# Kernel tuning notes

Measured on AMD Instinct MI355X. Metric: run time of the kernel, lower is better.

Reference implementation:

```python
import jax, jax.numpy as jnp
import numpy as np
import math


def setup_inputs() -> dict:
    key = jax.random.key(0)
    ks = jax.random.split(key, 7)
    d_input, d_state, d_output = 256, 256, 256
    B_, S_ = 8, 4096
    x = jax.random.normal(ks[0], (B_, S_, d_input), dtype=jnp.float32)
    log_lambda_real = jax.random.normal(ks[1], (d_state,), dtype=jnp.float32)
    lambda_imag = jax.random.normal(ks[2], (d_state,), dtype=jnp.float32)
    dt = jnp.clip(0.01 + jax.random.normal(ks[3], (d_state,), dtype=jnp.float32) * 0.01, 0.005, 0.1)
    log_dt = jnp.log(dt)
    B = jax.random.normal(ks[4], (d_state, d_input), dtype=jnp.float32) / d_state ** 0.5
    C_real = jax.random.normal(ks[5], (d_output, d_state), dtype=jnp.float32) / d_state ** 0.5
    C_imag = jax.random.normal(ks[6], (d_output, d_state), dtype=jnp.float32) / d_state ** 0.5
    return {"x": x, "log_lambda_real": log_lambda_real, "lambda_imag": lambda_imag,
            "log_dt": log_dt, "B": B, "C_real": C_real, "C_imag": C_imag}


def reference(x, log_lambda_real, lambda_imag, log_dt, B, C_real, C_imag):
    batch, seq_len, _ = x.shape
    # continuous-time poles and step sizes
    Lambda = -jnp.exp(log_lambda_real) + 1j * lambda_imag            # [N] complex
    dt = jnp.clip(jnp.exp(log_dt), 0.005, 0.1)                       # [N]
    # bilinear discretization
    denom = 1.0 - 0.5 * dt * Lambda                                  # [N] complex
    A_bar = (1.0 + 0.5 * dt * Lambda) / denom                        # [N] complex
    B_bar = (dt / denom)[:, None] * B                                # [N, d_in] complex
    # project input into state space: u[b,s,n] (complex)
    u = jnp.matmul(x, B_bar.real.T) + 1j * jnp.matmul(x, B_bar.imag.T)  # [B,S,N]
    # kernel A^0 .. A^{L-1} via cumprod (faithful to original)
    A_poles = jnp.broadcast_to(A_bar[:, None], (A_bar.shape[0], seq_len))  # [N,S]
    A_cp = jnp.cumprod(A_poles, axis=1)
    A_powers = jnp.concatenate([jnp.ones_like(A_cp[:, :1]), A_cp[:, :-1]], axis=1)  # [N,S]
    # FFT causal convolution
    n_fft = 2 ** math.ceil(math.log2(seq_len * 2 - 1))
    u_t = jnp.swapaxes(u, 1, 2)                                      # [B,N,S]
    u_f = jnp.fft.fft(u_t, n=n_fft, axis=-1)                          # [B,N,F]
    A_f = jnp.fft.fft(A_powers, n=n_fft, axis=-1)                     # [N,F]
    h = jnp.fft.ifft(u_f * A_f[None], n=n_fft, axis=-1)[..., :seq_len]  # [B,N,S]
    h = jnp.swapaxes(h, 1, 2)                                         # [B,S,N]
    # output projection, keep real part
    C_c = C_real + 1j * C_imag                                        # [d_out,N]
    return jnp.matmul(h, C_c.T).real                                  # [B,S,d_out]
```

## Files before the change

kernel.cpp:

```cpp
#include <hip/hip_runtime.h>
#include <hip/hip_bf16.h>

#define BB 8
#define SS 4096
#define NN 256
#define CHUNK 32
#define NCH (SS/CHUNK)

#define WS_FINR_B ((size_t)0)
#define WS_FINI_B ((size_t)1 << 20)
#define WS_CP_B   ((size_t)2 << 20)
#define WS_BP_B   (((size_t)2 << 20) + (256u << 10))

typedef __bf16 bf16_t;
typedef bf16_t bf16x8 __attribute__((ext_vector_type(8)));
typedef float  f32x4  __attribute__((ext_vector_type(4)));
typedef unsigned int u32x4 __attribute__((ext_vector_type(4)));

__device__ inline bf16_t f2b(float f) {
    __hip_bfloat16 h = __float2bfloat16(f);
    return __builtin_bit_cast(bf16_t, h);
}
__device__ inline float b2f_lo(unsigned v) {
    unsigned u = v << 16; return __builtin_bit_cast(float, u);
}
__device__ inline float b2f_hi(unsigned v) {
    unsigned u = v & 0xffff0000u; return __builtin_bit_cast(float, u);
}
__device__ inline unsigned pack2(float lo, float hi) {
    unsigned a = (unsigned)__builtin_bit_cast(unsigned short, f2b(lo));
    unsigned b = (unsigned)__builtin_bit_cast(unsigned short, f2b(hi));
    return a | (b << 16);
}
__device__ inline bf16x8 cvt8(f32x4 a, f32x4 b) {
    bf16x8 o;
    o[0]=f2b(a[0]); o[1]=f2b(a[1]); o[2]=f2b(a[2]); o[3]=f2b(a[3]);
    o[4]=f2b(b[0]); o[5]=f2b(b[1]); o[6]=f2b(b[2]); o[7]=f2b(b[3]);
    return o;
}

__device__ inline void ssm_consts(const float* llr, const float* li, const float* ldt,
                                  int n, float& Ar, float& Ai, float& sr, float& si) {
    float lr = -expf(llr[n]);
    float im = li[n];
    float dt = expf(ldt[n]);
    dt = fminf(fmaxf(dt, 0.005f), 0.1f);
    float hr = 0.5f * dt * lr, hi = 0.5f * dt * im;
    float dr = 1.f - hr, di = -hi;
    float inv = 1.f / (dr*dr + di*di);
    Ar = ((1.f + hr)*dr + hi*di) * inv;
    Ai = (hi*dr - (1.f + hr)*di) * inv;
    sr = dt * dr * inv;
    si = -dt * di * inv;
}

__global__ __launch_bounds__(256) void kprep(const float* __restrict__ Bw,
                                             const float* __restrict__ Cr,
                                             const float* __restrict__ Ci,
                                             u32x4* __restrict__ Cpack,
                                             u32x4* __restrict__ Bpack) {
    int t = threadIdx.x, bid = blockIdx.x;
    const float* src;
    float sign;
    u32x4* dst;
    int ks;
    if (bid < 16) { ks = bid;      src = (ks < 8) ? Cr : Ci; sign = (ks < 8) ? 1.f : -1.f; dst = Cpack; }
    else          { ks = bid - 16; src = Bw;                 sign = 1.f;                   dst = Bpack; }
    int ksl = ks & 7;
    #pragma unroll
    for (int jj = 0; jj < 4; ++jj) {
        int s = t + 256 * jj;
        int ot = s >> 6, lane = s & 63;
        int o  = ot*16 + (lane & 15);
        int kb = ksl*32 + (lane >> 4)*8;
        bf16x8 v;
        #pragma unroll
        for (int e = 0; e < 8; ++e) v[e] = f2b(sign * src[o*256 + kb + e]);
        dst[(ks*16 + ot)*64 + lane] = __builtin_bit_cast(u32x4, v);
    }
}


__global__ __launch_bounds__(256, 2) void kA(
    const float* __restrict__ X,
    const float* __restrict__ llr,
    const float* __restrict__ li,
    const float* __restrict__ ldt,
    const u32x4* __restrict__ Bpack,
    float* __restrict__ finr,
    float* __restrict__ fini,
    float* __restrict__ out)
{
    __shared__ __align__(16) char hlds[65536];
    int t = threadIdx.x;
    int bid = blockIdx.x;
    int m0 = bid * 64;
    int b = bid >> 6;
    int cbase = (bid & 63) * 2;
    int w = t >> 6, lane = t & 63, q = lane >> 4, r = lane & 15;

    f32x4 acc[4][4] = {};
    for (int kk = 0; kk < 4; ++kk) {
        #pragma unroll
        for (int ss = 0; ss < 2; ++ss) {
            int s = t + 256 * ss;
            int m = s >> 3, kg = s & 7;
            const f32x4* px = (const f32x4*)(X + (size_t)(m0 + m)*256 + kk*64 + kg*8);
            *(bf16x8*)(hlds + 32768 + m*128 + ((kg ^ (m & 7)) << 4)) = cvt8(px[0], px[1]);
        }
        __syncthreads();
        bf16x8 bp[2][4], xf[2][4];
        #pragma unroll
        for (int kb = 0; kb < 2; ++kb) {
            #pragma unroll
            for (int nt = 0; nt < 4; ++nt)
                bp[kb][nt] = __builtin_bit_cast(bf16x8,
                    Bpack[((kk*2 + kb)*16 + w*4 + nt)*64 + lane]);
            #pragma unroll
            for (int mt = 0; mt < 4; ++mt) {
                int m = mt*16 + r;
                xf[kb][mt] = *(const bf16x8*)(hlds + 32768 + m*128 +
                                              (((kb*4 + q) ^ (m & 7)) << 4));
            }
        }
        #pragma unroll
        for (int kb = 0; kb < 2; ++kb)
            #pragma unroll
            for (int nt = 0; nt < 4; ++nt)
                #pragma unroll
                for (int mt = 0; mt < 4; ++mt)
                    acc[nt][mt] = __builtin_amdgcn_mfma_f32_16x16x32_bf16(
                        bp[kb][nt], xf[kb][mt], acc[nt][mt], 0, 0, 0);
        __syncthreads();
    }
    #pragma unroll
    for (int nt = 0; nt < 4; ++nt) {
        int n0 = w*64 + nt*16 + q*4;
        #pragma unroll
        for (int mt = 0; mt < 4; ++mt) {
            int m = mt*16 + r;
            uint2 d;
            d.x = pack2(acc[nt][mt][0], acc[nt][mt][1]);
            d.y = pack2(acc[nt][mt][2], acc[nt][mt][3]);
            *(uint2*)(hlds + m*512 + (((n0 >> 3) ^ ((m >> 1) & 31)) << 4) + (n0 & 7)*2) = d;
        }
    }
    __syncthreads();

    {
        int p = t & 127, ch = t >> 7;
        int cb = cbase + ch;
        float Ar0,Ai0,sr0,si0, Ar1,Ai1,sr1,si1;
        ssm_consts(llr, li, ldt, 2*p,   Ar0, Ai0, sr0, si0);
        ssm_consts(llr, li, ldt, 2*p+1, Ar1, Ai1, sr1, si1);
        float hr0=0.f, hi0=0.f, hr1=0.f, hi1=0.f;
        #pragma unroll
        for (int i2 = 0; i2 < 16; ++i2) {
            int row = ch*32 + i2*2;
            char* a = hlds + row*512 + (((p >> 2) ^ ((row >> 1) & 31)) << 4) + (p & 3)*4;
            unsigned v0 = *(unsigned*)a;
            unsigned v1 = *(unsigned*)(a + 512);
            float x0 = b2f_lo(v0), x1 = b2f_hi(v0);
            float t0r = fmaf(Ar0, hr0, fmaf(-Ai0, hi0, sr0*x0));
            float t0i = fmaf(Ar0, hi0, fmaf( Ai0, hr0, si0*x0));
            float t1r = fmaf(Ar1, hr1, fmaf(-Ai1, hi1, sr1*x1));
            float t1i = fmaf(Ar1, hi1, fmaf( Ai1, hr1, si1*x1));
            hr0=t0r; hi0=t0i; hr1=t1r; hi1=t1i;
            *(unsigned*)a           = pack2(hr0, hr1);
            *(unsigned*)(a + 32768) = pack2(hi0, hi1);
            x0 = b2f_lo(v1); x1 = b2f_hi(v1);
            t0r = fmaf(Ar0, hr0, fmaf(-Ai0, hi0, sr0*x0));
            t0i = fmaf(Ar0, hi0, fmaf( Ai0, hr0, si0*x0));
            t1r = fmaf(Ar1, hr1, fmaf(-Ai1, hi1, sr1*x1));
            t1i = fmaf(Ar1, hi1, fmaf( Ai1, hr1, si1*x1));
            hr0=t0r; hi0=t0i; hr1=t1r; hi1=t1i;
            *(unsigned*)(a + 512)         = pack2(hr0, hr1);
            *(unsigned*)(a + 32768 + 512) = pack2(hi0, hi1);
        }
        int f0 = (b*NCH + cb)*NN + 2*p;
        finr[f0] = hr0; finr[f0+1] = hr1;
        fini[f0] = hi0; fini[f0+1] = hi1;
    }
    __syncthreads();

    char* dst = (char*)out + ((size_t)bid << 16);
    #pragma unroll
    for (int jj = 0; jj < 16; ++jj)
        *(u32x4*)(dst + jj*4096 + t*16) = *(const u32x4*)(hlds + jj*4096 + t*16);
}

__global__ __launch_bounds__(256, 2) void kB(
    const float* __restrict__ llr,
    const float* __restrict__ li,
    const float* __restrict__ ldt,
    const u32x4* __restrict__ Cpack,
    const float* __restrict__ finr,
    const float* __restrict__ fini,
    float* __restrict__ out)
{
    __shared__ __align__(16) char hlds[65536];
    int t = threadIdx.x;
    int bid = blockIdx.x;
    int m0 = bid * 64;
    int b = bid >> 6;
    int cbase = (bid & 63) * 2;
    int w = t >> 6, lane = t & 63, q = lane >> 4, r = lane & 15;

    const char* src = (const char*)out + ((size_t)bid << 16);
    u32x4 img[16];
    #pragma unroll
    for (int jj = 0; jj < 16; ++jj)
        img[jj] = *(const u32x4*)(src + jj*4096 + t*16);

    int p = t & 127, ch = t >> 7;
    int cb = cbase + ch;
    float Ar0,Ai0,sr0,si0, Ar1,Ai1,sr1,si1;
    ssm_consts(llr, li, ldt, 2*p,   Ar0, Ai0, sr0, si0);
    ssm_consts(llr, li, ldt, 2*p+1, Ar1, Ai1, sr1, si1);
    float g0r=0.f, g0i=0.f, g1r=0.f, g1i=0.f;
    if (cb > 0) {
        float P0r=Ar0, P0i=Ai0, P1r=Ar1, P1i=Ai1;
        #pragma unroll
        for (int i = 0; i < 5; ++i) {
            float u0 = P0r*P0r - P0i*P0i; P0i = 2.f*P0r*P0i; P0r = u0;
            float u1 = P1r*P1r - P1i*P1i; P1i = 2.f*P1r*P1i; P1r = u1;
        }
        float c0r=0.f, c0i=0.f, c1r=0.f, c1i=0.f;
        #pragma unroll 4
        for (int j = 0; j < cb; ++j) {
            int ff = (b*NCH + j)*NN + 2*p;
            float2 fr = *(const float2*)(finr + ff);
            float2 fi = *(const float2*)(fini + ff);
            float n0r = fmaf(P0r, c0r, fmaf(-P0i, c0i, fr.x));
            float n0i = fmaf(P0r, c0i, fmaf( P0i, c0r, fi.x));
            float n1r = fmaf(P1r, c1r, fmaf(-P1i, c1i, fr.y));
            float n1i = fmaf(P1r, c1i, fmaf( P1i, c1r, fi.y));
            c0r=n0r; c0i=n0i; c1r=n1r; c1i=n1i;
        }
        g0r = Ar0*c0r - Ai0*c0i; g0i = Ar0*c0i + Ai0*c0r;
        g1r = Ar1*c1r - Ai1*c1i; g1i = Ar1*c1i + Ai1*c1r;
    }

    #pragma unroll
    for (int jj = 0; jj < 16; ++jj)
        *(u32x4*)(hlds + jj*4096 + t*16) = img[jj];
    __syncthreads();

    if (cb > 0) {
        #pragma unroll
        for (int i2 = 0; i2 < 16; ++i2) {
            int row = ch*32 + i2*2;
            char* a = hlds + row*512 + (((p >> 2) ^ ((row >> 1) & 31)) << 4) + (p & 3)*4;
            unsigned ur0 = *(unsigned*)a;
            unsigned ur1 = *(unsigned*)(a + 512);
            unsigned ui0 = *(unsigned*)(a + 32768);
            unsigned ui1 = *(unsigned*)(a + 32768 + 512);
            *(unsigned*)a           = pack2(b2f_lo(ur0) + g0r, b2f_hi(ur0) + g1r);
            *(unsigned*)(a + 32768) = pack2(b2f_lo(ui0) + g0i, b2f_hi(ui0) + g1i);
            { float t0 = Ar0*g0r - Ai0*g0i; g0i = fmaf(Ar0, g0i, Ai0*g0r); g0r = t0;
              float t1 = Ar1*g1r - Ai1*g1i; g1i = fmaf(Ar1, g1i, Ai1*g1r); g1r = t1; }
            *(unsigned*)(a + 512)         = pack2(b2f_lo(ur1) + g0r, b2f_hi(ur1) + g1r);
            *(unsigned*)(a + 32768 + 512) = pack2(b2f_lo(ui1) + g0i, b2f_hi(ui1) + g1i);
            { float t0 = Ar0*g0r - Ai0*g0i; g0i = fmaf(Ar0, g0i, Ai0*g0r); g0r = t0;
              float t1 = Ar1*g1r - Ai1*g1i; g1i = fmaf(Ar1, g1i, Ai1*g1r); g1r = t1; }
        }
    }
    __syncthreads();

    f32x4 acc2[4][4] = {};
    #pragma unroll
    for (int ks = 0; ks < 16; ++ks) {
        int base = (ks & 8) ? 32768 : 0;
        int kin = ks & 7;
        bf16x8 af[4];
        #pragma unroll
        for (int mt = 0; mt < 4; ++mt) {
            int row = mt*16 + r;
            af[mt] = *(const bf16x8*)(hlds + base + row*512 +
                     (((kin*4 + q) ^ ((row >> 1) & 31)) << 4));
        }
        #pragma unroll
        for (int nt = 0; nt < 4; ++nt) {
            bf16x8 cf = __builtin_bit_cast(bf16x8, Cpack[(ks*16 + w*4 + nt)*64 + lane]);
            #pragma unroll
            for (int mt = 0; mt < 4; ++mt)
                acc2[mt][nt] = __builtin_amdgcn_mfma_f32_16x16x32_bf16(
                    af[mt], cf, acc2[mt][nt], 0, 0, 0);
        }
    }
    #pragma unroll
    for (int mt = 0; mt < 4; ++mt)
        #pragma unroll
        for (int nt = 0; nt < 4; ++nt)
            #pragma unroll
            for (int reg = 0; reg < 4; ++reg)
                out[(size_t)(m0 + mt*16 + q*4 + reg)*NN + w*64 + nt*16 + r] =
                    acc2[mt][nt][reg];
}

extern "C" void kernel_launch(void* const* d_in, const int* in_sizes, int n_in,
                              void* d_out, int out_size, void* d_ws, size_t ws_size,
                              hipStream_t stream) {
    const float* x   = (const float*)d_in[0];
    const float* llr = (const float*)d_in[1];
    const float* li  = (const float*)d_in[2];
    const float* ldt = (const float*)d_in[3];
    const float* Bw  = (const float*)d_in[4];
    const float* Cr  = (const float*)d_in[5];
    const float* Ci  = (const float*)d_in[6];

    char* wsb = (char*)d_ws;
    float* finr  = (float*)(wsb + WS_FINR_B);
    float* fini  = (float*)(wsb + WS_FINI_B);
    u32x4* Cpack = (u32x4*)(wsb + WS_CP_B);
    u32x4* Bpack = (u32x4*)(wsb + WS_BP_B);
    float* outp  = (float*)d_out;

    kprep<<<24, 256, 0, stream>>>(Bw, Cr, Ci, Cpack, Bpack);
    kA<<<512, 256, 0, stream>>>(x, llr, li, ldt, Bpack, finr, fini, outp);
    kB<<<512, 256, 0, stream>>>(llr, li, ldt, Cpack, finr, fini, outp);
}
```

Baseline: 131.7 us.

## Fuse chunk scan and output kernels using inter-block flag synchronization

Merges the two main kernels into one. Each block publishes its chunk-final states with atomic stores and a release flag, then spins on the flags of earlier blocks in the same batch before applying the carry and the output projection. This removes the round trip of the 64KB per-block intermediate image through global memory and one kernel launch. It relies on all 512 blocks being co-resident, or on blocks being dispatched in order, to avoid deadlock, and it adds spin-wait latency along the chunk dependency chain.

```diff
diff --git a/kernel.cpp b/kernel.cpp
--- a/kernel.cpp
+++ b/kernel.cpp
@@ -7,15 +7,17 @@
 #define CHUNK 32
 #define NCH (SS/CHUNK)
 
-#define WS_FINR_B ((size_t)0)
-#define WS_FINI_B ((size_t)1 << 20)
-#define WS_CP_B   ((size_t)2 << 20)
-#define WS_BP_B   (((size_t)2 << 20) + (256u << 10))
+#define WS_FINU_B ((size_t)0)
+#define WS_FINV_B ((size_t)1 << 20)
+#define WS_FLAG_B ((size_t)2 << 20)
+#define WS_CP_B   (((size_t)2 << 20) + 65536)
+#define WS_BP_B   (((size_t)2 << 20) + 65536 + 262144)
 
 typedef __bf16 bf16_t;
 typedef bf16_t bf16x8 __attribute__((ext_vector_type(8)));
 typedef float  f32x4  __attribute__((ext_vector_type(4)));
 typedef unsigned int u32x4 __attribute__((ext_vector_type(4)));
+typedef unsigned long long u64_t;
 
 __device__ inline bf16_t f2b(float f) {
     __hip_bfloat16 h = __float2bfloat16(f);
@@ -58,8 +60,10 @@
                                              const float* __restrict__ Cr,
                                              const float* __restrict__ Ci,
                                              u32x4* __restrict__ Cpack,
-                                             u32x4* __restrict__ Bpack) {
+                                             u32x4* __restrict__ Bpack,
+                                             int* __restrict__ flags) {
     int t = threadIdx.x, bid = blockIdx.x;
+    if (bid == 0) { flags[t] = 0; flags[t + 256] = 0; }
     const float* src;
     float sign;
     u32x4* dst;
@@ -81,14 +85,16 @@
 }
 
 
-__global__ __launch_bounds__(256, 2) void kA(
+__global__ __launch_bounds__(256, 2) void kfused(
     const float* __restrict__ X,
     const float* __restrict__ llr,
     const float* __restrict__ li,
     const float* __restrict__ ldt,
     const u32x4* __restrict__ Bpack,
-    float* __restrict__ finr,
-    float* __restrict__ fini,
+    const u32x4* __restrict__ Cpack,
+    u64_t* __restrict__ finu,
+    u64_t* __restrict__ finv,
+    int* __restrict__ flags,
     float* __restrict__ out)
 {
     __shared__ __align__(16) char hlds[65536];
@@ -96,7 +102,8 @@
     int bid = blockIdx.x;
     int m0 = bid * 64;
     int b = bid >> 6;
-    int cbase = (bid & 63) * 2;
+    int d = bid & 63;
+    int cbase = d * 2;
     int w = t >> 6, lane = t & 63, q = lane >> 4, r = lane & 15;
 
     f32x4 acc[4][4] = {};
@@ -139,20 +146,20 @@
         #pragma unroll
         for (int mt = 0; mt < 4; ++mt) {
             int m = mt*16 + r;
-            uint2 d;
-            d.x = pack2(acc[nt][mt][0], acc[nt][mt][1]);
-            d.y = pack2(acc[nt][mt][2], acc[nt][mt][3]);
-            *(uint2*)(hlds + m*512 + (((n0 >> 3) ^ ((m >> 1) & 31)) << 4) + (n0 & 7)*2) = d;
+            uint2 dd;
+            dd.x = pack2(acc[nt][mt][0], acc[nt][mt][1]);
+            dd.y = pack2(acc[nt][mt][2], acc[nt][mt][3]);
+            *(uint2*)(hlds + m*512 + (((n0 >> 3) ^ ((m >> 1) & 31)) << 4) + (n0 & 7)*2) = dd;
         }
     }
     __syncthreads();
 
+    int p = t & 127, ch = t >> 7;
+    int cb = cbase + ch;
+    float Ar0,Ai0,sr0,si0, Ar1,Ai1,sr1,si1;
+    ssm_consts(llr, li, ldt, 2*p,   Ar0, Ai0, sr0, si0);
+    ssm_consts(llr, li, ldt, 2*p+1, Ar1, Ai1, sr1, si1);
     {
-        int p = t & 127, ch = t >> 7;
-        int cb = cbase + ch;
-        float Ar0,Ai0,sr0,si0, Ar1,Ai1,sr1,si1;
-        ssm_consts(llr, li, ldt, 2*p,   Ar0, Ai0, sr0, si0);
-        ssm_consts(llr, li, ldt, 2*p+1, Ar1, Ai1, sr1, si1);
         float hr0=0.f, hi0=0.f, hr1=0.f, hi1=0.f;
         #pragma unroll
         for (int i2 = 0; i2 < 16; ++i2) {
@@ -177,48 +184,28 @@
             *(unsigned*)(a + 512)         = pack2(hr0, hr1);
             *(unsigned*)(a + 32768 + 512) = pack2(hi0, hi1);
         }
-        int f0 = (b*NCH + cb)*NN + 2*p;
-        finr[f0] = hr0; finr[f0+1] = hr1;
-        fini[f0] = hi0; fini[f0+1] = hi1;
+        float2 fr2; fr2.x = hr0; fr2.y = hr1;
+        float2 fi2; fi2.x = hi0; fi2.y = hi1;
+        size_t fidx = (size_t)(b*NCH + cb)*128 + p;
+        __hip_atomic_store(finu + fidx, __builtin_bit_cast(u64_t, fr2),
+                           __ATOMIC_RELAXED, __HIP_MEMORY_SCOPE_AGENT);
+        __hip_atomic_store(finv + fidx, __builtin_bit_cast(u64_t, fi2),
+                           __ATOMIC_RELAXED, __HIP_MEMORY_SCOPE_AGENT);
     }
     __syncthreads();
-
-    char* dst = (char*)out + ((size_t)bid << 16);
-    #pragma unroll
-    for (int jj = 0; jj < 16; ++jj)
-        *(u32x4*)(dst + jj*4096 + t*16) = *(const u32x4*)(hlds + jj*4096 + t*16);
-}
-
-__global__ __launch_bounds__(256, 2) void kB(
-    const float* __restrict__ llr,
-    const float* __restrict__ li,
-    const float* __restrict__ ldt,
-    const u32x4* __restrict__ Cpack,
-    const float* __restrict__ finr,
-    const float* __restrict__ fini,
-    float* __restrict__ out)
-{
-    __shared__ __align__(16) char hlds[65536];
-    int t = threadIdx.x;
-    int bid = blockIdx.x;
-    int m0 = bid * 64;
-    int b = bid >> 6;
-    int cbase = (bid & 63) * 2;
-    int w = t >> 6, lane = t & 63, q = lane >> 4, r = lane & 15;
-
-    const char* src = (const char*)out + ((size_t)bid << 16);
-    u32x4 img[16];
-    #pragma unroll
-    for (int jj = 0; jj < 16; ++jj)
-        img[jj] = *(const u32x4*)(src + jj*4096 + t*16);
-
-    int p = t & 127, ch = t >> 7;
-    int cb = cbase + ch;
-    float Ar0,Ai0,sr0,si0, Ar1,Ai1,sr1,si1;
-    ssm_consts(llr, li, ldt, 2*p,   Ar0, Ai0, sr0, si0);
-    ssm_consts(llr, li, ldt, 2*p+1, Ar1, Ai1, sr1, si1);
-    float g0r=0.f, g0i=0.f, g1r=0.f, g1i=0.f;
+    if (t == 0)
+        __hip_atomic_store(flags + bid, 1, __ATOMIC_RELEASE, __HIP_MEMORY_SCOPE_AGENT);
+
     if (cb > 0) {
+        if (d > 0) {
+            int fi_ = b*64 + ((lane < d) ? lane : 0);
+            while (true) {
+                int fl = __hip_atomic_load(flags + fi_, __ATOMIC_ACQUIRE,
+                                           __HIP_MEMORY_SCOPE_AGENT);
+                if (__all(fl != 0)) break;
+                __builtin_amdgcn_s_sleep(16);
+            }
+        }
         float P0r=Ar0, P0i=Ai0, P1r=Ar1, P1i=Ai1;
         #pragma unroll
         for (int i = 0; i < 5; ++i) {
@@ -228,25 +215,18 @@
         float c0r=0.f, c0i=0.f, c1r=0.f, c1i=0.f;
         #pragma unroll 4
         for (int j = 0; j < cb; ++j) {
-            int ff = (b*NCH + j)*NN + 2*p;
-            float2 fr = *(const float2*)(finr + ff);
-            float2 fi = *(const float2*)(fini + ff);
+            u64_t vr = finu[(size_t)(b*NCH + j)*128 + p];
+            u64_t vi = finv[(size_t)(b*NCH + j)*128 + p];
+            float2 fr = __builtin_bit_cast(float2, vr);
+            float2 fi = __builtin_bit_cast(float2, vi);
             float n0r = fmaf(P0r, c0r, fmaf(-P0i, c0i, fr.x));
             float n0i = fmaf(P0r, c0i, fmaf( P0i, c0r, fi.x));
             float n1r = fmaf(P1r, c1r, fmaf(-P1i, c1i, fr.y));
             float n1i = fmaf(P1r, c1i, fmaf( P1i, c1r, fi.y));
             c0r=n0r; c0i=n0i; c1r=n1r; c1i=n1i;
         }
-        g0r = Ar0*c0r - Ai0*c0i; g0i = Ar0*c0i + Ai0*c0r;
-        g1r = Ar1*c1r - Ai1*c1i; g1i = Ar1*c1i + Ai1*c1r;
-    }
-
-    #pragma unroll
-    for (int jj = 0; jj < 16; ++jj)
-        *(u32x4*)(hlds + jj*4096 + t*16) = img[jj];
-    __syncthreads();
-
-    if (cb > 0) {
+        float g0r = Ar0*c0r - Ai0*c0i, g0i = Ar0*c0i + Ai0*c0r;
+        float g1r = Ar1*c1r - Ai1*c1i, g1i = Ar1*c1i + Ai1*c1r;
         #pragma unroll
         for (int i2 = 0; i2 < 16; ++i2) {
             int row = ch*32 + i2*2;
@@ -310,13 +290,14 @@
     const float* Ci  = (const float*)d_in[6];
 
     char* wsb = (char*)d_ws;
-    float* finr  = (float*)(wsb + WS_FINR_B);
-    float* fini  = (float*)(wsb + WS_FINI_B);
+    u64_t* finu  = (u64_t*)(wsb + WS_FINU_B);
+    u64_t* finv  = (u64_t*)(wsb + WS_FINV_B);
+    int*   flags = (int*)(wsb + WS_FLAG_B);
     u32x4* Cpack = (u32x4*)(wsb + WS_CP_B);
     u32x4* Bpack = (u32x4*)(wsb + WS_BP_B);
     float* outp  = (float*)d_out;
 
-    kprep<<<24, 256, 0, stream>>>(Bw, Cr, Ci, Cpack, Bpack);
-    kA<<<512, 256, 0, stream>>>(x, llr, li, ldt, Bpack, finr, fini, outp);
-    kB<<<512, 256, 0, stream>>>(llr, li, ldt, Cpack, finr, fini, outp);
-}
+    kprep<<<24, 256, 0, stream>>>(Bw, Cr, Ci, Cpack, Bpack, flags);
+    kfused<<<512, 256, 0, stream>>>(x, llr, li, ldt, Bpack, Cpack,
+                                    finu, finv, flags, outp);
+}
```

Measured after the change: 156.7 us. +19.0%, slower.

## Pass real bf16 projection instead of complex scan image between kernels

Applied to the files above, without the earlier changes.

kA now writes only the bf16 input projection u (32KB per block) to a workspace buffer and computes chunk-final states without storing the complex scan. kB reloads u, computes the carry-in prefix, then reruns the chunk scan starting from the carry and writes real and imaginary states into LDS for the output GEMM. This halves the intermediate global traffic and shrinks kA's LDS so it can raise occupancy to 3 blocks. In exchange the scan is computed twice, once in each kernel.

```diff
diff --git a/kernel.cpp b/kernel.cpp
--- a/kernel.cpp
+++ b/kernel.cpp
@@ -9,8 +9,9 @@
 
 #define WS_FINR_B ((size_t)0)
 #define WS_FINI_B ((size_t)1 << 20)
-#define WS_CP_B   ((size_t)2 << 20)
-#define WS_BP_B   (((size_t)2 << 20) + (256u << 10))
+#define WS_VIMG_B ((size_t)2 << 20)
+#define WS_CP_B   ((size_t)18 << 20)
+#define WS_BP_B   (((size_t)18 << 20) + 262144)
 
 typedef __bf16 bf16_t;
 typedef bf16_t bf16x8 __attribute__((ext_vector_type(8)));
@@ -81,7 +82,7 @@
 }
 
 
-__global__ __launch_bounds__(256, 2) void kA(
+__global__ __launch_bounds__(256, 3) void kA(
     const float* __restrict__ X,
     const float* __restrict__ llr,
     const float* __restrict__ li,
@@ -89,6 +90,113 @@
     const u32x4* __restrict__ Bpack,
     float* __restrict__ finr,
     float* __restrict__ fini,
+    char* __restrict__ vimg)
+{
+    __shared__ __align__(16) char hlds[40960];
+    int t = threadIdx.x;
+    int bid = blockIdx.x;
+    int m0 = bid * 64;
+    int b = bid >> 6;
+    int cbase = (bid & 63) * 2;
+    int w = t >> 6, lane = t & 63, q = lane >> 4, r = lane & 15;
+
+    f32x4 acc[4][4] = {};
+    for (int kk = 0; kk < 4; ++kk) {
+        #pragma unroll
+        for (int ss = 0; ss < 2; ++ss) {
+            int s = t + 256 * ss;
+            int m = s >> 3, kg = s & 7;
+            const f32x4* px = (const f32x4*)(X + (size_t)(m0 + m)*256 + kk*64 + kg*8);
+            *(bf16x8*)(hlds + 32768 + m*128 + ((kg ^ (m & 7)) << 4)) = cvt8(px[0], px[1]);
+        }
+        __syncthreads();
+        bf16x8 bp[2][4], xf[2][4];
+        #pragma unroll
+        for (int kb = 0; kb < 2; ++kb) {
+            #pragma unroll
+            for (int nt = 0; nt < 4; ++nt)
+                bp[kb][nt] = __builtin_bit_cast(bf16x8,
+                    Bpack[((kk*2 + kb)*16 + w*4 + nt)*64 + lane]);
+            #pragma unroll
+            for (int mt = 0; mt < 4; ++mt) {
+                int m = mt*16 + r;
+                xf[kb][mt] = *(const bf16x8*)(hlds + 32768 + m*128 +
+                                              (((kb*4 + q) ^ (m & 7)) << 4));
+            }
+        }
+        #pragma unroll
+        for (int kb = 0; kb < 2; ++kb)
+            #pragma unroll
+            for (int nt = 0; nt < 4; ++nt)
+                #pragma unroll
+                for (int mt = 0; mt < 4; ++mt)
+                    acc[nt][mt] = __builtin_amdgcn_mfma_f32_16x16x32_bf16(
+                        bp[kb][nt], xf[kb][mt], acc[nt][mt], 0, 0, 0);
+        __syncthreads();
+    }
+    #pragma unroll
+    for (int nt = 0; nt < 4; ++nt) {
+        int n0 = w*64 + nt*16 + q*4;
+        #pragma unroll
+        for (int mt = 0; mt < 4; ++mt) {
+            int m = mt*16 + r;
+            uint2 dd;
+            dd.x = pack2(acc[nt][mt][0], acc[nt][mt][1]);
+            dd.y = pack2(acc[nt][mt][2], acc[nt][mt][3]);
+            *(uint2*)(hlds + m*512 + (((n0 >> 3) ^ ((m >> 1) & 31)) << 4) + (n0 & 7)*2) = dd;
+        }
+    }
+    __syncthreads();
+
+    {
+        char* dst = vimg + ((size_t)bid << 15);
+        #pragma unroll
+        for (int jj = 0; jj < 8; ++jj)
+            *(u32x4*)(dst + jj*4096 + t*16) = *(const u32x4*)(hlds + jj*4096 + t*16);
+    }
+
+    {
+        int p = t & 127, ch = t >> 7;
+        int cb = cbase + ch;
+        float Ar0,Ai0,sr0,si0, Ar1,Ai1,sr1,si1;
+        ssm_consts(llr, li, ldt, 2*p,   Ar0, Ai0, sr0, si0);
+        ssm_consts(llr, li, ldt, 2*p+1, Ar1, Ai1, sr1, si1);
+        float hr0=0.f, hi0=0.f, hr1=0.f, hi1=0.f;
+        #pragma unroll
+        for (int i2 = 0; i2 < 16; ++i2) {
+            int row = ch*32 + i2*2;
+            const char* a = hlds + row*512 + (((p >> 2) ^ ((row >> 1) & 31)) << 4) + (p & 3)*4;
+            unsigned v0 = *(const unsigned*)a;
+            unsigned v1 = *(const unsigned*)(a + 512);
+            float x0 = b2f_lo(v0), x1 = b2f_hi(v0);
+            float t0r = fmaf(Ar0, hr0, fmaf(-Ai0, hi0, sr0*x0));
+            float t0i = fmaf(Ar0, hi0, fmaf( Ai0, hr0, si0*x0));
+            float t1r = fmaf(Ar1, hr1, fmaf(-Ai1, hi1, sr1*x1));
+            float t1i = fmaf(Ar1, hi1, fmaf( Ai1, hr1, si1*x1));
+            hr0=t0r; hi0=t0i; hr1=t1r; hi1=t1i;
+            x0 = b2f_lo(v1); x1 = b2f_hi(v1);
+            t0r = fmaf(Ar0, hr0, fmaf(-Ai0, hi0, sr0*x0));
+            t0i = fmaf(Ar0, hi0, fmaf( Ai0, hr0, si0*x0));
+            t1r = fmaf(Ar1, hr1, fmaf(-Ai1, hi1, sr1*x1));
+            t1i = fmaf(Ar1, hi1, fmaf( Ai1, hr1, si1*x1));
+            hr0=t0r; hi0=t0i; hr1=t1r; hi1=t1i;
+        }
+        int f0 = (b*NCH + cb)*NN + 2*p;
+        float2 fr2; fr2.x = hr0; fr2.y = hr1;
+        float2 fi2; fi2.x = hi0; fi2.y = hi1;
+        *(float2*)(finr + f0) = fr2;
+        *(float2*)(fini + f0) = fi2;
+    }
+}
+
+__global__ __launch_bounds__(256, 2) void kB(
+    const float* __restrict__ llr,
+    const float* __restrict__ li,
+    const float* __restrict__ ldt,
+    const u32x4* __restrict__ Cpack,
+    const float* __restrict__ finr,
+    const float* __restrict__ fini,
+    const char* __restrict__ vimg,
     float* __restrict__ out)
 {
     __shared__ __align__(16) char hlds[65536];
@@ -99,61 +207,45 @@
     int cbase = (bid & 63) * 2;
     int w = t >> 6, lane = t & 63, q = lane >> 4, r = lane & 15;
 
-    f32x4 acc[4][4] = {};
-    for (int kk = 0; kk < 4; ++kk) {
-        #pragma unroll
-        for (int ss = 0; ss < 2; ++ss) {
-            int s = t + 256 * ss;
-            int m = s >> 3, kg = s & 7;
-            const f32x4* px = (const f32x4*)(X + (size_t)(m0 + m)*256 + kk*64 + kg*8);
-            *(bf16x8*)(hlds + 32768 + m*128 + ((kg ^ (m & 7)) << 4)) = cvt8(px[0], px[1]);
-        }
-        __syncthreads();
-        bf16x8 bp[2][4], xf[2][4];
-        #pragma unroll
-        for (int kb = 0; kb < 2; ++kb) {
-            #pragma unroll
-            for (int nt = 0; nt < 4; ++nt)
-                bp[kb][nt] = __builtin_bit_cast(bf16x8,
-                    Bpack[((kk*2 + kb)*16 + w*4 + nt)*64 + lane]);
-            #pragma unroll
-            for (int mt = 0; mt < 4; ++mt) {
-                int m = mt*16 + r;
-                xf[kb][mt] = *(const bf16x8*)(hlds + 32768 + m*128 +
-                                              (((kb*4 + q) ^ (m & 7)) << 4));
-            }
-        }
-        #pragma unroll
-        for (int kb = 0; kb < 2; ++kb)
-            #pragma unroll
-            for (int nt = 0; nt < 4; ++nt)
-                #pragma unroll
-                for (int mt = 0; mt < 4; ++mt)
-                    acc[nt][mt] = __builtin_amdgcn_mfma_f32_16x16x32_bf16(
-                        bp[kb][nt], xf[kb][mt], acc[nt][mt], 0, 0, 0);
-        __syncthreads();
-    }
-    #pragma unroll
-    for (int nt = 0; nt < 4; ++nt) {
-        int n0 = w*64 + nt*16 + q*4;
-        #pragma unroll
-        for (int mt = 0; mt < 4; ++mt) {
-            int m = mt*16 + r;
-            uint2 d;
-            d.x = pack2(acc[nt][mt][0], acc[nt][mt][1]);
-            d.y = pack2(acc[nt][mt][2], acc[nt][mt][3]);
-            *(uint2*)(hlds + m*512 + (((n0 >> 3) ^ ((m >> 1) & 31)) << 4) + (n0 & 7)*2) = d;
-        }
-    }
+    const char* src = vimg + ((size_t)bid << 15);
+    u32x4 img[8];
+    #pragma unroll
+    for (int jj = 0; jj < 8; ++jj)
+        img[jj] = *(const u32x4*)(src + jj*4096 + t*16);
+
+    int p = t & 127, ch = t >> 7;
+    int cb = cbase + ch;
+    float Ar0,Ai0,sr0,si0, Ar1,Ai1,sr1,si1;
+    ssm_consts(llr, li, ldt, 2*p,   Ar0, Ai0, sr0, si0);
+    ssm_consts(llr, li, ldt, 2*p+1, Ar1, Ai1, sr1, si1);
+    float c0r=0.f, c0i=0.f, c1r=0.f, c1i=0.f;
+    if (cb > 0) {
+        float P0r=Ar0, P0i=Ai0, P1r=Ar1, P1i=Ai1;
+        #pragma unroll
+        for (int i = 0; i < 5; ++i) {
+            float u0 = P0r*P0r - P0i*P0i; P0i = 2.f*P0r*P0i; P0r = u0;
+            float u1 = P1r*P1r - P1i*P1i; P1i = 2.f*P1r*P1i; P1r = u1;
+        }
+        #pragma unroll 4
+        for (int j = 0; j < cb; ++j) {
+            int ff = (b*NCH + j)*NN + 2*p;
+            float2 fr = *(const float2*)(finr + ff);
+            float2 fi = *(const float2*)(fini + ff);
+            float n0r = fmaf(P0r, c0r, fmaf(-P0i, c0i, fr.x));
+            float n0i = fmaf(P0r, c0i, fmaf( P0i, c0r, fi.x));
+            float n1r = fmaf(P1r, c1r, fmaf(-P1i, c1i, fr.y));
+            float n1i = fmaf(P1r, c1i, fmaf( P1i, c1r, fi.y));
+            c0r=n0r; c0i=n0i; c1r=n1r; c1i=n1i;
+        }
+    }
+
+    #pragma unroll
+    for (int jj = 0; jj < 8; ++jj)
+        *(u32x4*)(hlds + jj*4096 + t*16) = img[jj];
     __syncthreads();
 
     {
-        int p = t & 127, ch = t >> 7;
-        int cb = cbase + ch;
-        float Ar0,Ai0,sr0,si0, Ar1,Ai1,sr1,si1;
-        ssm_consts(llr, li, ldt, 2*p,   Ar0, Ai0, sr0, si0);
-        ssm_consts(llr, li, ldt, 2*p+1, Ar1, Ai1, sr1, si1);
-        float hr0=0.f, hi0=0.f, hr1=0.f, hi1=0.f;
+        float hr0=c0r, hi0=c0i, hr1=c1r, hi1=c1i;
         #pragma unroll
         for (int i2 = 0; i2 < 16; ++i2) {
             int row = ch*32 + i2*2;
@@ -177,93 +269,6 @@
             *(unsigned*)(a + 512)         = pack2(hr0, hr1);
             *(unsigned*)(a + 32768 + 512) = pack2(hi0, hi1);
         }
-        int f0 = (b*NCH + cb)*NN + 2*p;
-        finr[f0] = hr0; finr[f0+1] = hr1;
-        fini[f0] = hi0; fini[f0+1] = hi1;
-    }
-    __syncthreads();
-
-    char* dst = (char*)out + ((size_t)bid << 16);
-    #pragma unroll
-    for (int jj = 0; jj < 16; ++jj)
-        *(u32x4*)(dst + jj*4096 + t*16) = *(const u32x4*)(hlds + jj*4096 + t*16);
-}
-
-__global__ __launch_bounds__(256, 2) void kB(
-    const float* __restrict__ llr,
-    const float* __restrict__ li,
-    const float* __restrict__ ldt,
-    const u32x4* __restrict__ Cpack,
-    const float* __restrict__ finr,
-    const float* __restrict__ fini,
-    float* __restrict__ out)
-{
-    __shared__ __align__(16) char hlds[65536];
-    int t = threadIdx.x;
-    int bid = blockIdx.x;
-    int m0 = bid * 64;
-    int b = bid >> 6;
-    int cbase = (bid & 63) * 2;
-    int w = t >> 6, lane = t & 63, q = lane >> 4, r = lane & 15;
-
-    const char* src = (const char*)out + ((size_t)bid << 16);
-    u32x4 img[16];
-    #pragma unroll
-    for (int jj = 0; jj < 16; ++jj)
-        img[jj] = *(const u32x4*)(src + jj*4096 + t*16);
-
-    int p = t & 127, ch = t >> 7;
-    int cb = cbase + ch;
-    float Ar0,Ai0,sr0,si0, Ar1,Ai1,sr1,si1;
-    ssm_consts(llr, li, ldt, 2*p,   Ar0, Ai0, sr0, si0);
-    ssm_consts(llr, li, ldt, 2*p+1, Ar1, Ai1, sr1, si1);
-    float g0r=0.f, g0i=0.f, g1r=0.f, g1i=0.f;
-    if (cb > 0) {
-        float P0r=Ar0, P0i=Ai0, P1r=Ar1, P1i=Ai1;
-        #pragma unroll
-        for (int i = 0; i < 5; ++i) {
-            float u0 = P0r*P0r - P0i*P0i; P0i = 2.f*P0r*P0i; P0r = u0;
-            float u1 = P1r*P1r - P1i*P1i; P1i = 2.f*P1r*P1i; P1r = u1;
-        }
-        float c0r=0.f, c0i=0.f, c1r=0.f, c1i=0.f;
-        #pragma unroll 4
-        for (int j = 0; j < cb; ++j) {
-            int ff = (b*NCH + j)*NN + 2*p;
-            float2 fr = *(const float2*)(finr + ff);
-            float2 fi = *(const float2*)(fini + ff);
-            float n0r = fmaf(P0r, c0r, fmaf(-P0i, c0i, fr.x));
-            float n0i = fmaf(P0r, c0i, fmaf( P0i, c0r, fi.x));
-            float n1r = fmaf(P1r, c1r, fmaf(-P1i, c1i, fr.y));
-            float n1i = fmaf(P1r, c1i, fmaf( P1i, c1r, fi.y));
-            c0r=n0r; c0i=n0i; c1r=n1r; c1i=n1i;
-        }
-        g0r = Ar0*c0r - Ai0*c0i; g0i = Ar0*c0i + Ai0*c0r;
-        g1r = Ar1*c1r - Ai1*c1i; g1i = Ar1*c1i + Ai1*c1r;
-    }
-
-    #pragma unroll
-    for (int jj = 0; jj < 16; ++jj)
-        *(u32x4*)(hlds + jj*4096 + t*16) = img[jj];
-    __syncthreads();
-
-    if (cb > 0) {
-        #pragma unroll
-        for (int i2 = 0; i2 < 16; ++i2) {
-            int row = ch*32 + i2*2;
-            char* a = hlds + row*512 + (((p >> 2) ^ ((row >> 1) & 31)) << 4) + (p & 3)*4;
-            unsigned ur0 = *(unsigned*)a;
-            unsigned ur1 = *(unsigned*)(a + 512);
-            unsigned ui0 = *(unsigned*)(a + 32768);
-            unsigned ui1 = *(unsigned*)(a + 32768 + 512);
-            *(unsigned*)a           = pack2(b2f_lo(ur0) + g0r, b2f_hi(ur0) + g1r);
-            *(unsigned*)(a + 32768) = pack2(b2f_lo(ui0) + g0i, b2f_hi(ui0) + g1i);
-            { float t0 = Ar0*g0r - Ai0*g0i; g0i = fmaf(Ar0, g0i, Ai0*g0r); g0r = t0;
-              float t1 = Ar1*g1r - Ai1*g1i; g1i = fmaf(Ar1, g1i, Ai1*g1r); g1r = t1; }
-            *(unsigned*)(a + 512)         = pack2(b2f_lo(ur1) + g0r, b2f_hi(ur1) + g1r);
-            *(unsigned*)(a + 32768 + 512) = pack2(b2f_lo(ui1) + g0i, b2f_hi(ui1) + g1i);
-            { float t0 = Ar0*g0r - Ai0*g0i; g0i = fmaf(Ar0, g0i, Ai0*g0r); g0r = t0;
-              float t1 = Ar1*g1r - Ai1*g1i; g1i = fmaf(Ar1, g1i, Ai1*g1r); g1r = t1; }
-        }
     }
     __syncthreads();
 
@@ -312,11 +317,12 @@
     char* wsb = (char*)d_ws;
     float* finr  = (float*)(wsb + WS_FINR_B);
     float* fini  = (float*)(wsb + WS_FINI_B);
+    char*  vimg  = wsb + WS_VIMG_B;
     u32x4* Cpack = (u32x4*)(wsb + WS_CP_B);
     u32x4* Bpack = (u32x4*)(wsb + WS_BP_B);
     float* outp  = (float*)d_out;
 
     kprep<<<24, 256, 0, stream>>>(Bw, Cr, Ci, Cpack, Bpack);
-    kA<<<512, 256, 0, stream>>>(x, llr, li, ldt, Bpack, finr, fini, outp);
-    kB<<<512, 256, 0, stream>>>(llr, li, ldt, Cpack, finr, fini, outp);
-}
+    kA<<<512, 256, 0, stream>>>(x, llr, li, ldt, Bpack, finr, fini, vimg);
+    kB<<<512, 256, 0, stream>>>(llr, li, ldt, Cpack, finr, fini, vimg, outp);
+}
```

Result: no change. 131.6 us (-0.0%).
